# Kernel tuning notes

Hardware: AMD Instinct MI355X
Metric: run time of the kernel (lower is better)

The kernel has to match this reference:

```python
import jax, jax.numpy as jnp
import numpy as np

NUM_HEADS = 16
NUM_HIDDENS = 1024
D_K = NUM_HIDDENS // NUM_HEADS
NEG_INF = -1.0e9


def setup_inputs() -> dict:
    key = jax.random.key(0)
    kx, kq, kk, kv, ko, kl = jax.random.split(key, 6)
    B, S, D = 2, 2048, NUM_HIDDENS
    scale = 1.0 / np.sqrt(D)
    return {
        "X": jax.random.normal(kx, (B, S, D), dtype=jnp.float32),
        "valid_lens": jax.random.randint(kl, (B,), 0, S, dtype=jnp.int64),
        "W_q": jax.random.normal(kq, (D, D), dtype=jnp.float32) * scale,
        "W_k": jax.random.normal(kk, (D, D), dtype=jnp.float32) * scale,
        "W_v": jax.random.normal(kv, (D, D), dtype=jnp.float32) * scale,
        "W_o": jax.random.normal(ko, (D, D), dtype=jnp.float32) * scale,
    }


def _split_heads(x):
    # [B, S, D] -> [B, H, S, d_k]
    B, S, _ = x.shape
    return x.reshape(B, S, NUM_HEADS, D_K).transpose(0, 2, 1, 3)


def reference(X, valid_lens, W_q, W_k, W_v, W_o):
    B, S, D = X.shape
    # nn.Linear(bias=False): y = x @ W.T  (W is [out, in])
    Q = _split_heads(jnp.einsum("bsd,ed->bse", X, W_q))  # [B,H,S,dk]
    K = _split_heads(jnp.einsum("bsd,ed->bse", X, W_k))
    V = _split_heads(jnp.einsum("bsd,ed->bse", X, W_v))

    scores = jnp.einsum("bhqd,bhkd->bhqk", Q, K) / jnp.sqrt(
        jnp.asarray(D_K, dtype=X.dtype)
    )  # [B,H,S,S]

    # key-position mask per batch: positions >= valid_len get -1e9
    mask = jnp.arange(S)[None, :] >= valid_lens[:, None]  # [B,S]
    scores = jnp.where(mask[:, None, None, :], jnp.asarray(NEG_INF, X.dtype), scores)

    attn = jax.nn.softmax(scores, axis=-1)  # dropout p=0 -> identity
    out = jnp.einsum("bhqk,bhkd->bhqd", attn, V)  # [B,H,S,dk]
    out = out.transpose(0, 2, 1, 3).reshape(B, S, D)
    return jnp.einsum("bsd,ed->bse", out, W_o)
```

## Files before the change

kernel.cpp:

```cpp
#include <hip/hip_runtime.h>
#include <stdint.h>

#define S_LEN 2048
#define BATCH 2
#define DMODEL 1024
#define NHEAD 16
#define DK 64
#define MROWS (BATCH * S_LEN)

typedef __attribute__((ext_vector_type(8))) short bf16x8;
typedef __attribute__((ext_vector_type(4))) float f32x4;
typedef __attribute__((ext_vector_type(16))) float f32x16;
typedef __attribute__((ext_vector_type(4))) short short4v;

#define VMCNT(N) asm volatile("s_waitcnt vmcnt(" #N ")" ::: "memory")

__device__ __forceinline__ short f2b(float f) {
    union { float f; uint32_t u; } c; c.f = f;
    uint32_t u = c.u;
    return (short)((u + 0x7fffu + ((u >> 16) & 1u)) >> 16);
}

__device__ __forceinline__ void gload16(const void* g, void* l) {
    __builtin_amdgcn_global_load_lds(
        (const __attribute__((address_space(1))) void*)g,
        (__attribute__((address_space(3))) void*)l, 16, 0, 0);
}

__global__ void cvt_kernel(const float* __restrict__ X, const float* __restrict__ Wq,
                           const float* __restrict__ Wk, const float* __restrict__ Wv,
                           const float* __restrict__ Wo,
                           short* __restrict__ Xb, short* __restrict__ Wqb,
                           short* __restrict__ Wkb, short* __restrict__ Wvb,
                           short* __restrict__ Wob) {
    const float* src; short* dst; int n4;
    switch (blockIdx.y) {
        case 0:  src = X;  dst = Xb;  n4 = MROWS * DMODEL / 4;  break;
        case 1:  src = Wq; dst = Wqb; n4 = DMODEL * DMODEL / 4; break;
        case 2:  src = Wk; dst = Wkb; n4 = DMODEL * DMODEL / 4; break;
        case 3:  src = Wv; dst = Wvb; n4 = DMODEL * DMODEL / 4; break;
        default: src = Wo; dst = Wob; n4 = DMODEL * DMODEL / 4; break;
    }
    for (int i = blockIdx.x * blockDim.x + threadIdx.x; i < n4;
         i += gridDim.x * blockDim.x) {
        float4 v = ((const float4*)src)[i];
        short4v o;
        o[0] = f2b(v.x); o[1] = f2b(v.y); o[2] = f2b(v.z); o[3] = f2b(v.w);
        ((short4v*)dst)[i] = o;
    }
}

template <int OUT_F32>
__global__ __launch_bounds__(256) void gemm_bt(
    const short* __restrict__ A,
    const short* __restrict__ Bt0, const short* __restrict__ Bt1,
    const short* __restrict__ Bt2,
    short* __restrict__ Cb0, short* __restrict__ Cb1, short* __restrict__ Cb2,
    float* __restrict__ Cf, int M, int N, int K) {
    __shared__ short sA[3][128 * 32];
    __shared__ short sB[3][128 * 32];

    const short* Bt = Bt0;
    short* Cb = Cb0;
    if (blockIdx.z == 1) { Bt = Bt1; Cb = Cb1; }
    else if (blockIdx.z == 2) { Bt = Bt2; Cb = Cb2; }

    const int tid = threadIdx.x;
    const int lane = tid & 63;
    const int wid = tid >> 6;
    const int wr = wid >> 1, wc = wid & 1;
    const int brow = blockIdx.y * 128;
    const int bcol = blockIdx.x * 128;
    const int lr = lane & 15;
    const int kh = (lane >> 4) << 3;
    const int swg = ((lr >> 1) & 3) << 3;
    const int khs = kh ^ swg;

    f32x4 acc[4][4] = {};

    const int idx0 = tid, idx1 = tid + 256;
    const int ar0 = idx0 >> 2, ak0 = ((idx0 & 3) << 3) ^ (((ar0 >> 1) & 3) << 3);
    const int ar1 = idx1 >> 2, ak1 = ((idx1 & 3) << 3) ^ (((ar1 >> 1) & 3) << 3);

    const short* gA0 = A + (size_t)(brow + ar0) * K + ak0;
    const short* gA1 = A + (size_t)(brow + ar1) * K + ak1;
    const short* gB0 = Bt + (size_t)(bcol + ar0) * K + ak0;
    const short* gB1 = Bt + (size_t)(bcol + ar1) * K + ak1;

#define G_STAGE(KT, PA, PB)                                   \
    do {                                                      \
        const int k0_ = (KT) << 5;                            \
        gload16(gA0 + k0_, (PA) + idx0 * 8);                  \
        gload16(gA1 + k0_, (PA) + idx1 * 8);                  \
        gload16(gB0 + k0_, (PB) + idx0 * 8);                  \
        gload16(gB1 + k0_, (PB) + idx1 * 8);                  \
    } while (0)

    const int nk = K >> 5;
    short* pA0 = &sA[0][0]; short* pA1 = &sA[1][0]; short* pA2 = &sA[2][0];
    short* pB0 = &sB[0][0]; short* pB1 = &sB[1][0]; short* pB2 = &sB[2][0];

    G_STAGE(0, pA0, pB0);
    G_STAGE(1, pA1, pB1);

    for (int kt = 0; kt < nk; ++kt) {
        if (kt == nk - 1) { VMCNT(0); } else { VMCNT(4); }
        __builtin_amdgcn_s_barrier();
        if (kt + 2 < nk) G_STAGE(kt + 2, pA2, pB2);

        bf16x8 a[4], b[4];
#pragma unroll
        for (int mt = 0; mt < 4; ++mt)
            a[mt] = *(const bf16x8*)&pA0[(wr * 64 + mt * 16 + lr) * 32 + khs];
#pragma unroll
        for (int nt = 0; nt < 4; ++nt)
            b[nt] = *(const bf16x8*)&pB0[(wc * 64 + nt * 16 + lr) * 32 + khs];
        __builtin_amdgcn_s_setprio(1);
#pragma unroll
        for (int mt = 0; mt < 4; ++mt)
#pragma unroll
            for (int nt = 0; nt < 4; ++nt)
                acc[mt][nt] = __builtin_amdgcn_mfma_f32_16x16x32_bf16(
                    a[mt], b[nt], acc[mt][nt], 0, 0, 0);
        __builtin_amdgcn_s_setprio(0);

        short* tA = pA0; pA0 = pA1; pA1 = pA2; pA2 = tA;
        short* tB = pB0; pB0 = pB1; pB1 = pB2; pB2 = tB;
    }
#undef G_STAGE

    const int rbase = (lane >> 4) << 2;
    const bool vtrans = (!OUT_F32) && (blockIdx.z == 2);
#pragma unroll
    for (int mt = 0; mt < 4; ++mt) {
#pragma unroll
        for (int nt = 0; nt < 4; ++nt) {
            if (vtrans) {
                int row0 = brow + wr * 64 + mt * 16 + rbase;
                int col = bcol + wc * 64 + nt * 16 + lr;
                int bb = row0 >> 11, key = row0 & 2047;
                int hh = col >> 6, d = col & 63;
                short4v pk;
#pragma unroll
                for (int j = 0; j < 4; ++j) pk[j] = f2b(acc[mt][nt][j]);
                *(short4v*)&Cb[((size_t)((bb * 16 + hh) * 64 + d)) * S_LEN + key] = pk;
            } else {
#pragma unroll
                for (int j = 0; j < 4; ++j) {
                    int row = brow + wr * 64 + mt * 16 + rbase + j;
                    int col = bcol + wc * 64 + nt * 16 + lr;
                    if (OUT_F32)
                        Cf[(size_t)row * N + col] = acc[mt][nt][j];
                    else
                        Cb[(size_t)row * N + col] = f2b(acc[mt][nt][j]);
                }
            }
        }
    }
}

__global__ __launch_bounds__(256, 3) void attn_kernel(
    const short* __restrict__ Q, const short* __restrict__ K,
    const short* __restrict__ Vt, short* __restrict__ O,
    const int* __restrict__ vlens) {
    __shared__ short sK[3][64 * 64];
    __shared__ short sV[3][64 * 64];

    const int tid = threadIdx.x;
    const int lane = tid & 63;
    const int w = tid >> 6;
    const int id = blockIdx.x;
    const int xcd = id & 7;
    const int r = id >> 3;
    const int b = (r >> 5) & 1;
    const int h = (xcd << 1) | (r & 1);
    const int qb = (r >> 1) & 15;
    const int rl_ = lane & 31;
    const int g = lane >> 5;
    const int sw = (lane & 7) << 3;

    int vl = vlens[b];
    if (vl < 0) vl = 0;
    if (vl > S_LEN) vl = S_LEN;
    const bool allm = (vl == 0);
    if (allm) vl = S_LEN;
    const int nT = (vl + 63) >> 6;
    const int nFull = ((vl & 63) == 0) ? nT : nT - 1;

    const size_t rowbase = (size_t)(b * S_LEN) * DMODEL + h * DK;
    const short* vt = Vt + ((size_t)((b * 16 + h) * 64)) * S_LEN;

    const int q = qb * 128 + w * 32 + rl_;
    const short* qA = Q + rowbase + (size_t)q * DMODEL;
    bf16x8 qf[4];
#pragma unroll
    for (int f = 0; f < 4; ++f)
        qf[f] = *(const bf16x8*)(qA + f * 16 + g * 8);
    if (allm) {
#pragma unroll
        for (int f = 0; f < 4; ++f)
#pragma unroll
            for (int i = 0; i < 8; ++i) qf[f][i] = 0;
    }

    f32x16 oac0 = {}, oac1 = {};
    float m_run = -1e30f, mc = -1e30f, l_run = 0.f;
    const float CEXP = 0.18033688011112042f;
    const float THRADD = 44.361419556f;

    int lofs[4];
#pragma unroll
    for (int f = 0; f < 4; ++f)
        lofs[f] = rl_ * 64 + (((f * 16) + g * 8) ^ sw);

    const int kr = tid >> 3;
    const int kc = (((tid & 7) ^ (kr & 7)) << 3);
    const short* kBase = K + rowbase + (size_t)kr * DMODEL + kc;
    const short* vBase = vt + (size_t)kr * S_LEN + kc;

#define A_STAGE(T, PK, PV)                                                      \
    do {                                                                        \
        const short* kg_ = kBase + (size_t)((T) * 64) * DMODEL;                 \
        gload16(kg_, (PK) + tid * 8);                                           \
        gload16(kg_ + (size_t)32 * DMODEL, (PK) + (tid + 256) * 8);             \
        const short* vg_ = vBase + (T) * 64;                                    \
        gload16(vg_, (PV) + tid * 8);                                           \
        gload16(vg_ + (size_t)32 * S_LEN, (PV) + (tid + 256) * 8);              \
    } while (0)

#define MK_FRAG(A0, A1, A2, A3)                                                 \
    ({ union { uint32_t u[4]; bf16x8 v; } _f;                                   \
       _f.u[0] = (A0); _f.u[1] = (A1); _f.u[2] = (A2); _f.u[3] = (A3); _f.v; })

#define TILE_BODY(MASKED_C, PK, PV)                                             \
    do {                                                                        \
        constexpr bool MASKED = MASKED_C;                                       \
        f32x16 s0 = {}, s1 = {};                                                \
        __builtin_amdgcn_s_setprio(1);                                          \
        _Pragma("unroll")                                                       \
        for (int f = 0; f < 4; ++f) {                                           \
            bf16x8 ka = *(const bf16x8*)&(PK)[lofs[f]];                         \
            bf16x8 kb2 = *(const bf16x8*)&(PK)[lofs[f] + 2048];                 \
            s0 = __builtin_amdgcn_mfma_f32_32x32x16_bf16(ka, qf[f], s0, 0, 0, 0); \
            s1 = __builtin_amdgcn_mfma_f32_32x32x16_bf16(kb2, qf[f], s1, 0, 0, 0); \
        }                                                                       \
        __builtin_amdgcn_s_setprio(0);                                          \
        if (MASKED) {                                                           \
            _Pragma("unroll")                                                   \
            for (int rg = 0; rg < 16; ++rg) {                                   \
                int key0 = t * 64 + (rg & 3) + 8 * (rg >> 2) + 4 * g;           \
                if (key0 >= vl) s0[rg] = -3.0e38f;                              \
                if (key0 + 32 >= vl) s1[rg] = -3.0e38f;                         \
            }                                                                   \
        }                                                                       \
        float x0 = fmaxf(fmaxf(s0[0], s0[1]), fmaxf(s0[2], s0[3]));             \
        float x1 = fmaxf(fmaxf(s0[4], s0[5]), fmaxf(s0[6], s0[7]));             \
        float x2 = fmaxf(fmaxf(s0[8], s0[9]), fmaxf(s0[10], s0[11]));           \
        float x3 = fmaxf(fmaxf(s0[12], s0[13]), fmaxf(s0[14], s0[15]));         \
        float x4 = fmaxf(fmaxf(s1[0], s1[1]), fmaxf(s1[2], s1[3]));             \
        float x5 = fmaxf(fmaxf(s1[4], s1[5]), fmaxf(s1[6], s1[7]));             \
        float x6 = fmaxf(fmaxf(s1[8], s1[9]), fmaxf(s1[10], s1[11]));           \
        float x7 = fmaxf(fmaxf(s1[12], s1[13]), fmaxf(s1[14], s1[15]));         \
        float px = fmaxf(fmaxf(fmaxf(x0, x1), fmaxf(x2, x3)),                   \
                         fmaxf(fmaxf(x4, x5), fmaxf(x6, x7)));                  \
        if (__any(px > m_run + THRADD)) {                                       \
            float mx = fmaxf(px, __shfl_xor(px, 32));                           \
            mx = fmaxf(mx, m_run);                                              \
            float scl = __builtin_exp2f((m_run - mx) * CEXP);                   \
            m_run = mx; mc = mx * CEXP;                                         \
            l_run *= scl;                                                       \
            _Pragma("unroll")                                                   \
            for (int i = 0; i < 16; ++i) { oac0[i] *= scl; oac1[i] *= scl; }    \
        }                                                                       \
        uint32_t P0[8], P1[8];                                                  \
        float ls = 0.f;                                                         \
        _Pragma("unroll")                                                       \
        for (int i = 0; i < 8; ++i) {                                           \
            float a0 = __builtin_exp2f(__builtin_fmaf(s0[2 * i], CEXP, -mc));   \
            float a1 = __builtin_exp2f(__builtin_fmaf(s0[2 * i + 1], CEXP, -mc)); \
            float b0 = __builtin_exp2f(__builtin_fmaf(s1[2 * i], CEXP, -mc));   \
            float b1 = __builtin_exp2f(__builtin_fmaf(s1[2 * i + 1], CEXP, -mc)); \
            ls += (a0 + a1) + (b0 + b1);                                        \
            asm("v_cvt_pk_bf16_f32 %0, %1, %2" : "=v"(P0[i]) : "v"(a0), "v"(a1)); \
            asm("v_cvt_pk_bf16_f32 %0, %1, %2" : "=v"(P1[i]) : "v"(b0), "v"(b1)); \
        }                                                                       \
        l_run += ls;                                                            \
        asm volatile("v_permlane32_swap_b32 %0, %1" : "+v"(P0[0]), "+v"(P0[2])); \
        asm volatile("v_permlane32_swap_b32 %0, %1" : "+v"(P0[1]), "+v"(P0[3])); \
        asm volatile("v_permlane32_swap_b32 %0, %1" : "+v"(P0[4]), "+v"(P0[6])); \
        asm volatile("v_permlane32_swap_b32 %0, %1" : "+v"(P0[5]), "+v"(P0[7])); \
        asm volatile("v_permlane32_swap_b32 %0, %1" : "+v"(P1[0]), "+v"(P1[2])); \
        asm volatile("v_permlane32_swap_b32 %0, %1" : "+v"(P1[1]), "+v"(P1[3])); \
        asm volatile("v_permlane32_swap_b32 %0, %1" : "+v"(P1[4]), "+v"(P1[6])); \
        asm volatile("v_permlane32_swap_b32 %0, %1" : "+v"(P1[5]), "+v"(P1[7])); \
        bf16x8 F0 = MK_FRAG(P0[0], P0[1], P0[2], P0[3]);                        \
        bf16x8 F1 = MK_FRAG(P0[4], P0[5], P0[6], P0[7]);                        \
        bf16x8 F2 = MK_FRAG(P1[0], P1[1], P1[2], P1[3]);                        \
        bf16x8 F3 = MK_FRAG(P1[4], P1[5], P1[6], P1[7]);                        \
        __builtin_amdgcn_s_setprio(1);                                          \
        {                                                                       \
            bf16x8 v0 = *(const bf16x8*)&(PV)[lofs[0]];                         \
            bf16x8 v1 = *(const bf16x8*)&(PV)[lofs[0] + 2048];                  \
            oac0 = __builtin_amdgcn_mfma_f32_32x32x16_bf16(v0, F0, oac0, 0, 0, 0); \
            oac1 = __builtin_amdgcn_mfma_f32_32x32x16_bf16(v1, F0, oac1, 0, 0, 0); \
            v0 = *(const bf16x8*)&(PV)[lofs[1]];                                \
            v1 = *(const bf16x8*)&(PV)[lofs[1] + 2048];                         \
            oac0 = __builtin_amdgcn_mfma_f32_32x32x16_bf16(v0, F1, oac0, 0, 0, 0); \
            oac1 = __builtin_amdgcn_mfma_f32_32x32x16_bf16(v1, F1, oac1, 0, 0, 0); \
            v0 = *(const bf16x8*)&(PV)[lofs[2]];                                \
            v1 = *(const bf16x8*)&(PV)[lofs[2] + 2048];                         \
            oac0 = __builtin_amdgcn_mfma_f32_32x32x16_bf16(v0, F2, oac0, 0, 0, 0); \
            oac1 = __builtin_amdgcn_mfma_f32_32x32x16_bf16(v1, F2, oac1, 0, 0, 0); \
            v0 = *(const bf16x8*)&(PV)[lofs[3]];                                \
            v1 = *(const bf16x8*)&(PV)[lofs[3] + 2048];                         \
            oac0 = __builtin_amdgcn_mfma_f32_32x32x16_bf16(v0, F3, oac0, 0, 0, 0); \
            oac1 = __builtin_amdgcn_mfma_f32_32x32x16_bf16(v1, F3, oac1, 0, 0, 0); \
        }                                                                       \
        __builtin_amdgcn_s_setprio(0);                                          \
    } while (0)

    short* pK0 = &sK[0][0]; short* pK1 = &sK[1][0]; short* pK2 = &sK[2][0];
    short* pV0 = &sV[0][0]; short* pV1 = &sV[1][0]; short* pV2 = &sV[2][0];

    A_STAGE(0, pK0, pV0);
    if (nT > 1) A_STAGE(1, pK1, pV1);

    for (int t = 0; t < nT; ++t) {
        if (t == nT - 1) { VMCNT(0); } else { VMCNT(4); }
        __builtin_amdgcn_s_barrier();
        if (t + 2 < nT) A_STAGE(t + 2, pK2, pV2);

        if (t < nFull) TILE_BODY(false, pK0, pV0);
        else TILE_BODY(true, pK0, pV0);

        short* tK = pK0; pK0 = pK1; pK1 = pK2; pK2 = tK;
        short* tV = pV0; pV0 = pV1; pV1 = pV2; pV2 = tV;
    }
#undef TILE_BODY
#undef A_STAGE
#undef MK_FRAG

    float lt = l_run + __shfl_xor(l_run, 32);
    float rl2 = 1.f / lt;

    short* orow = O + rowbase + (size_t)q * DMODEL;
#pragma unroll
    for (int r2 = 0; r2 < 4; ++r2) {
        short4v pk0, pk1;
#pragma unroll
        for (int j = 0; j < 4; ++j) {
            pk0[j] = f2b(oac0[r2 * 4 + j] * rl2);
            pk1[j] = f2b(oac1[r2 * 4 + j] * rl2);
        }
        int d0 = r2 * 8 + 4 * g;
        *(short4v*)&orow[d0] = pk0;
        *(short4v*)&orow[32 + d0] = pk1;
    }
}

extern "C" void kernel_launch(void* const* d_in, const int* in_sizes, int n_in,
                              void* d_out, int out_size, void* d_ws, size_t ws_size,
                              hipStream_t stream) {
    const float* X = (const float*)d_in[0];
    const int* vlens = (const int*)d_in[1];
    const float* Wq = (const float*)d_in[2];
    const float* Wk = (const float*)d_in[3];
    const float* Wv = (const float*)d_in[4];
    const float* Wo = (const float*)d_in[5];
    float* out = (float*)d_out;

    short* Xb = (short*)d_ws;
    short* Wqb = Xb + (size_t)MROWS * DMODEL;
    short* Wkb = Wqb + (size_t)DMODEL * DMODEL;
    short* Wvb = Wkb + (size_t)DMODEL * DMODEL;
    short* Wob = Wvb + (size_t)DMODEL * DMODEL;
    short* Qb = Wob + (size_t)DMODEL * DMODEL;
    short* Kb = Qb + (size_t)MROWS * DMODEL;
    short* Vtb = Kb + (size_t)MROWS * DMODEL;
    short* Ob = Vtb + (size_t)MROWS * DMODEL;

    cvt_kernel<<<dim3(512, 5), 256, 0, stream>>>(X, Wq, Wk, Wv, Wo, Xb, Wqb, Wkb,
                                                 Wvb, Wob);
    gemm_bt<0><<<dim3(8, 32, 3), 256, 0, stream>>>(Xb, Wqb, Wkb, Wvb, Qb, Kb, Vtb,
                                                   nullptr, MROWS, DMODEL, DMODEL);
    attn_kernel<<<dim3(512), 256, 0, stream>>>(Qb, Kb, Vtb, Ob, vlens);
    gemm_bt<1><<<dim3(8, 32, 1), 256, 0, stream>>>(Ob, Wob, Wob, Wob, nullptr,
                                                   nullptr, nullptr, out, MROWS,
                                                   DMODEL, DMODEL);
}
```

Before: 107.3 us.

## Deepen attention K/V prefetch to four LDS stages and change swizzle

Grows the K/V shared-memory ring from three to four buffers, so tile loads are issued three iterations ahead. The vmcnt waits are adjusted to match, and buffers are indexed by t&3 instead of rotating pointers. The LDS XOR swizzle also mixes in row bits 3-4 to cut bank conflicts on fragment reads. In exchange, LDS use rises to 64KB per block and launch bounds drop occupancy to 2 blocks per CU.

New measurement: 105.4 us. Within noise of the previous version (-1.8%).

```diff
diff --git a/kernel.cpp b/kernel.cpp
--- a/kernel.cpp
+++ b/kernel.cpp
@@ -159,12 +159,12 @@
     }
 }
 
-__global__ __launch_bounds__(256, 3) void attn_kernel(
+__global__ __launch_bounds__(256, 2) void attn_kernel(
     const short* __restrict__ Q, const short* __restrict__ K,
     const short* __restrict__ Vt, short* __restrict__ O,
     const int* __restrict__ vlens) {
-    __shared__ short sK[3][64 * 64];
-    __shared__ short sV[3][64 * 64];
+    __shared__ short sK[4][64 * 64];
+    __shared__ short sV[4][64 * 64];
 
     const int tid = threadIdx.x;
     const int lane = tid & 63;
@@ -177,7 +177,6 @@
     const int qb = (r >> 1) & 15;
     const int rl_ = lane & 31;
     const int g = lane >> 5;
-    const int sw = (lane & 7) << 3;
 
     int vl = vlens[b];
     if (vl < 0) vl = 0;
@@ -208,15 +207,21 @@
     const float CEXP = 0.18033688011112042f;
     const float THRADD = 44.361419556f;
 
+    const int rsw = (((rl_ & 7) ^ ((rl_ >> 3) & 3)) << 3);
     int lofs[4];
 #pragma unroll
     for (int f = 0; f < 4; ++f)
-        lofs[f] = rl_ * 64 + (((f * 16) + g * 8) ^ sw);
+        lofs[f] = rl_ * 64 + ((f * 16 + g * 8) ^ rsw);
 
     const int kr = tid >> 3;
-    const int kc = (((tid & 7) ^ (kr & 7)) << 3);
+    const int kc = (((tid & 7) ^ (kr & 7) ^ ((kr >> 3) & 3)) << 3);
     const short* kBase = K + rowbase + (size_t)kr * DMODEL + kc;
     const short* vBase = vt + (size_t)kr * S_LEN + kc;
+
+    short* const sK0 = &sK[0][0];
+    short* const sV0 = &sV[0][0];
+#define KBUF(i) (sK0 + (i) * 4096)
+#define VBUF(i) (sV0 + (i) * 4096)
 
 #define A_STAGE(T, PK, PV)                                                      \
     do {                                                                        \
@@ -319,26 +324,28 @@
         __builtin_amdgcn_s_setprio(0);                                          \
     } while (0)
 
-    short* pK0 = &sK[0][0]; short* pK1 = &sK[1][0]; short* pK2 = &sK[2][0];
-    short* pV0 = &sV[0][0]; short* pV1 = &sV[1][0]; short* pV2 = &sV[2][0];
-
-    A_STAGE(0, pK0, pV0);
-    if (nT > 1) A_STAGE(1, pK1, pV1);
+    A_STAGE(0, KBUF(0), VBUF(0));
+    if (nT > 1) A_STAGE(1, KBUF(1), VBUF(1));
+    if (nT > 2) A_STAGE(2, KBUF(2), VBUF(2));
 
     for (int t = 0; t < nT; ++t) {
-        if (t == nT - 1) { VMCNT(0); } else { VMCNT(4); }
+        const int rem = nT - 1 - t;
+        if (rem >= 2) { VMCNT(8); }
+        else if (rem == 1) { VMCNT(4); }
+        else { VMCNT(0); }
         __builtin_amdgcn_s_barrier();
-        if (t + 2 < nT) A_STAGE(t + 2, pK2, pV2);
-
-        if (t < nFull) TILE_BODY(false, pK0, pV0);
-        else TILE_BODY(true, pK0, pV0);
-
-        short* tK = pK0; pK0 = pK1; pK1 = pK2; pK2 = tK;
-        short* tV = pV0; pV0 = pV1; pV1 = pV2; pV2 = tV;
+        if (t + 3 < nT) A_STAGE(t + 3, KBUF((t + 3) & 3), VBUF((t + 3) & 3));
+
+        short* curK = KBUF(t & 3);
+        short* curV = VBUF(t & 3);
+        if (t < nFull) TILE_BODY(false, curK, curV);
+        else TILE_BODY(true, curK, curV);
     }
 #undef TILE_BODY
 #undef A_STAGE
 #undef MK_FRAG
+#undef KBUF
+#undef VBUF
 
     float lt = l_run + __shfl_xor(l_run, 32);
     float rl2 = 1.f / lt;
```
